# Kernel optimization log

Measured on AMD Instinct MI355X. Metric: run time of the kernel, lower is better.

The kernel has to match this reference:

```python
import jax, jax.numpy as jnp
import numpy as np

A = -0.75  # PyTorch bicubic coefficient (a=-0.75)


def _cubic_taps(n):
    # output coord i maps to src = i/2 - 0.25 (align_corners=False, scale=2)
    i = np.arange(2 * n)
    src = i / 2.0 - 0.25
    base = np.floor(src).astype(np.int64)
    t = src - base
    offs = np.array([-1, 0, 1, 2])
    idx = np.clip(base[:, None] + offs[None, :], 0, n - 1)  # (2n,4) replicate border
    d = np.abs(t[:, None] - offs[None, :])
    w = np.where(d <= 1.0,
                 (A + 2) * d ** 3 - (A + 3) * d ** 2 + 1.0,
                 A * d ** 3 - 5 * A * d ** 2 + 8 * A * d - 4 * A)
    return jnp.asarray(idx), jnp.asarray(w.astype(np.float32))


def _upsample2_bicubic(x):
    B, C, H, W = x.shape
    ih, wh = _cubic_taps(H)
    iw, ww = _cubic_taps(W)
    x = (x[:, :, ih, :] * wh[None, None, :, :, None]).sum(3)   # (B,C,2H,W)
    x = (x[:, :, :, iw] * ww[None, None, None, :, :]).sum(4)   # (B,C,2H,2W)
    return x


def _conv2d(x, w, b, pad):
    y = jax.lax.conv_general_dilated(x, w, (1, 1), ((pad, pad), (pad, pad)),
                                     dimension_numbers=('NCHW', 'OIHW', 'NCHW'))
    return y + b[None, :, None, None]


def _instance_norm(x, w, b, eps=1e-5):
    m = x.mean(axis=(2, 3), keepdims=True)
    v = x.var(axis=(2, 3), keepdims=True)
    return (x - m) * jax.lax.rsqrt(v + eps) * w[None, :, None, None] + b[None, :, None, None]


def _prelu(x, a):
    return jnp.where(x >= 0, x, a * x)


def _unfold5(x):
    # 5x5 neighborhoods, pad=2 -> (B, C, 25, H, W); row-major kernel tap order
    B, C, H, W = x.shape
    xp = jnp.pad(x, ((0, 0), (0, 0), (2, 2), (2, 2)))
    return jnp.stack([xp[:, :, i:i + H, j:j + W] for i in range(5) for j in range(5)], axis=2)


def _forward(input, feature, conv1_w, conv1_b, in1_w, in1_b, prelu1_a,
             conv2_w, conv2_b, in2_w, in2_b, prelu2_a,
             res_w, res_b, feat_w, feat_b, pac_w, pac_b):
    # main mapping: conv-IN-PReLU x2
    y = _prelu(_instance_norm(_conv2d(input, conv1_w, conv1_b, 1), in1_w, in1_b), prelu1_a)
    y = _prelu(_instance_norm(_conv2d(y, conv2_w, conv2_b, 1), in2_w, in2_b), prelu2_a)
    # residual 1x1 mapping (in_channels != out_channels)
    y = y + _conv2d(input, res_w, res_b, 0)
    y = _upsample2_bicubic(y)                               # (B,O,2H,2W)
    # PAC guidance: gaussian kernel from 1x1-mapped feature, normalized over window
    g = _conv2d(feature, feat_w, feat_b, 0)                 # (B,O,2H,2W)
    gcols = _unfold5(g)                                     # (B,O,25,2H,2W)
    diff2 = ((gcols - g[:, :, None]) ** 2).sum(axis=1)      # (B,25,2H,2W)
    kern = jnp.exp(-0.5 * diff2)
    kern = kern / kern.sum(axis=1, keepdims=True)           # normalize_kernel=True
    xcols = _unfold5(y)                                     # (B,O,25,2H,2W)
    O, Ci = pac_w.shape[0], pac_w.shape[1]
    out = jnp.einsum('ocp,bcphw,bphw->bohw', pac_w.reshape(O, Ci, 25), xcols, kern)
    return out + pac_b[None, :, None, None]


def setup_inputs() -> dict:
    key = jax.random.key(0)
    ks = jax.random.split(key, 8)
    Cin, Cout, Cf = 256, 128, 128
    B, H, W = 2, 48, 48
    f32 = jnp.float32

    def w(k, shape, fan_in):
        return jax.random.normal(k, shape, f32) / np.float32(np.sqrt(fan_in))

    return {
        'input': jax.random.normal(ks[0], (B, Cin, H, W), f32),
        'feature': jax.random.normal(ks[1], (B, Cf, 2 * H, 2 * W), f32),
        'conv1_w': w(ks[2], (Cout, Cin, 3, 3), Cin * 9), 'conv1_b': jnp.zeros((Cout,), f32),
        'in1_w': jnp.ones((Cout,), f32), 'in1_b': jnp.zeros((Cout,), f32),
        'prelu1_a': jnp.asarray(0.25, f32),
        'conv2_w': w(ks[3], (Cout, Cout, 3, 3), Cout * 9), 'conv2_b': jnp.zeros((Cout,), f32),
        'in2_w': jnp.ones((Cout,), f32), 'in2_b': jnp.zeros((Cout,), f32),
        'prelu2_a': jnp.asarray(0.25, f32),
        'res_w': w(ks[4], (Cout, Cin, 1, 1), Cin), 'res_b': jnp.zeros((Cout,), f32),
        'feat_w': w(ks[5], (Cout, Cf, 1, 1), Cf), 'feat_b': jnp.zeros((Cout,), f32),
        'pac_w': w(ks[6], (Cout, Cout, 5, 5), Cout * 25), 'pac_b': jnp.zeros((Cout,), f32),
    }


def reference(input, feature, conv1_w, conv1_b, in1_w, in1_b, prelu1_a,
              conv2_w, conv2_b, in2_w, in2_b, prelu2_a,
              res_w, res_b, feat_w, feat_b, pac_w, pac_b):
    return _forward(input, feature, conv1_w, conv1_b, in1_w, in1_b, prelu1_a,
                    conv2_w, conv2_b, in2_w, in2_b, prelu2_a,
                    res_w, res_b, feat_w, feat_b, pac_w, pac_b)
```

## Files before the change

### kernel.cpp

```cpp
#include <hip/hip_runtime.h>
#include <hip/hip_bf16.h>

typedef __attribute__((ext_vector_type(8))) short bf16x8;
typedef __attribute__((ext_vector_type(4))) float f32x4;

constexpr int B   = 2;
constexpr int CIN = 256;
constexpr int CO  = 128;
constexpr int H = 48, W = 48;
constexpr int H2 = 96, W2 = 96;
constexpr int NPIX1 = H * W;
constexpr int NPIX2 = H2 * W2;
constexpr int NS = 4;

__device__ inline ushort f2bf(float v)
{
  __hip_bfloat16 h = __float2bfloat16(v);
  return *reinterpret_cast<ushort*>(&h);
}

__global__ __launch_bounds__(256) void prep_weights_kernel(
    const float* __restrict__ pac_w, const float* __restrict__ conv1_w,
    const float* __restrict__ conv2_w, const float* __restrict__ feat_w,
    const float* __restrict__ res_w,
    ushort* __restrict__ wbb, ushort* __restrict__ wt1, ushort* __restrict__ wt2,
    ushort* __restrict__ fwb, ushort* __restrict__ wrb)
{
  int blk = blockIdx.x, tid = threadIdx.x;
  if (blk < 1600) {
    int idx = blk * 256 + tid;
    int c = idx & 127, o = (idx >> 7) & 127, p = idx >> 14;
    wbb[idx] = f2bf(pac_w[((size_t)o * CO + c) * 25 + p]);
  } else if (blk < 2752) {
    int idx = (blk - 1600) * 256 + tid;
    int ci = idx & 255, o = (idx >> 8) & 127, tap = idx >> 15;
    wt1[idx] = f2bf(conv1_w[((size_t)o * CIN + ci) * 9 + tap]);
  } else if (blk < 3328) {
    int idx = (blk - 2752) * 256 + tid;
    int ci = idx & 127, o = (idx >> 7) & 127, tap = idx >> 14;
    wt2[idx] = f2bf(conv2_w[((size_t)o * CO + ci) * 9 + tap]);
  } else if (blk < 3392) {
    int idx = (blk - 3328) * 256 + tid;
    fwb[idx] = f2bf(feat_w[idx]);
  } else {
    int idx = (blk - 3392) * 256 + tid;
    wrb[idx] = f2bf(res_w[idx]);
  }
}

__global__ __launch_bounds__(256) void cvt_in_t_kernel(
    const float* __restrict__ in, ushort* __restrict__ outh)
{
  int blk = blockIdx.x;
  int cg = blk & 7;
  int pc = (blk >> 3) % 36;
  int b  = blk / (8 * 36);
  int c0 = cg * 32, pix0 = pc * 64;
  int tid = threadIdx.x;
  __shared__ float lt[32][65];
#pragma unroll
  for (int r = 0; r < 8; r++) {
    int c_l = r * 4 + (tid >> 6), px = tid & 63;
    lt[c_l][px] = in[((size_t)b * CIN + c0 + c_l) * NPIX1 + pix0 + px];
  }
  __syncthreads();
  int c_l = tid & 31;
#pragma unroll
  for (int r = 0; r < 8; r++) {
    int px = r * 8 + (tid >> 5);
    outh[((size_t)b * NPIX1 + pix0 + px) * CIN + c0 + c_l] = f2bf(lt[c_l][px]);
  }
}

__global__ __launch_bounds__(256) void cvt_feat_t_kernel(
    const float* __restrict__ in, ushort* __restrict__ outh)
{
  int blk = blockIdx.x;
  int cg = blk & 3;
  int pc = (blk >> 2) % 144;
  int b  = blk / (4 * 144);
  int c0 = cg * 32, pix0 = pc * 64;
  int tid = threadIdx.x;
  __shared__ float lt[32][65];
#pragma unroll
  for (int r = 0; r < 8; r++) {
    int c_l = r * 4 + (tid >> 6), px = tid & 63;
    lt[c_l][px] = in[((size_t)b * CO + c0 + c_l) * NPIX2 + pix0 + px];
  }
  __syncthreads();
  int c_l = tid & 31;
#pragma unroll
  for (int r = 0; r < 8; r++) {
    int px = r * 8 + (tid >> 5);
    outh[((size_t)b * NPIX2 + pix0 + px) * CO + c0 + c_l] = f2bf(lt[c_l][px]);
  }
}

template<int CIg>
__global__ __launch_bounds__(256, 4) void conv3_mfma_kernel(
    const ushort* __restrict__ xh,
    const ushort* __restrict__ wt,
    float* __restrict__ pout)
{
  constexpr int CS = CIg / NS;
  constexpr int G  = CS / 8;
  constexpr int KC = CS / 32;
  int blk = blockIdx.x;
  int tile = blk % 36;
  int s = (blk / 36) & 3;
  int b = blk / 144;
  int th = tile / 3, tw = tile % 3;
  int h0 = th * 4, w0 = tw * 16;
  int tid = threadIdx.x, lane = tid & 63, wv = tid >> 6;
  int l15 = lane & 15, l4 = (lane >> 4) & 3;

  __shared__ ushort xt[108 * CS];
  for (int q = tid; q < 108 * G; q += 256) {
    int pixi = q / G, g = q & (G - 1);
    int rh = pixi / 18, rw = pixi - rh * 18;
    int hg = h0 - 1 + rh, wg = w0 - 1 + rw;
    uint4 v{0u, 0u, 0u, 0u};
    if (hg >= 0 && hg < H && wg >= 0 && wg < W)
      v = *(const uint4*)(xh + (size_t)(b * NPIX1 + hg * W + wg) * CIg + s * CS + g * 8);
    *(uint4*)(xt + pixi * CS + ((g ^ (pixi & (G - 1))) * 8)) = v;
  }
  __syncthreads();

  int wo = wv * 32;
  const ushort* wbase = wt + (size_t)(wo + l15) * CIg + s * CS + l4 * 8;

  f32x4 acc0[4], acc1[4];
#pragma unroll
  for (int nf = 0; nf < 4; nf++) {
    acc0[nf] = {0.f, 0.f, 0.f, 0.f};
    acc1[nf] = {0.f, 0.f, 0.f, 0.f};
  }

  bf16x8 aC0[KC], aC1[KC], aN0[KC], aN1[KC];
#pragma unroll
  for (int kc = 0; kc < KC; kc++) {
    aC0[kc] = *(const bf16x8*)(wbase + kc * 32);
    aC1[kc] = *(const bf16x8*)(wbase + 16 * CIg + kc * 32);
  }

#pragma unroll 1
  for (int tap = 0; tap < 9; ++tap) {
    if (tap < 8) {
      const ushort* wn = wbase + (size_t)(tap + 1) * 128 * CIg;
#pragma unroll
      for (int kc = 0; kc < KC; kc++) {
        aN0[kc] = *(const bf16x8*)(wn + kc * 32);
        aN1[kc] = *(const bf16x8*)(wn + 16 * CIg + kc * 32);
      }
    }
    int kh = (tap >= 6) ? 2 : ((tap >= 3) ? 1 : 0);
    int kw = tap - kh * 3;
#pragma unroll
    for (int kc = 0; kc < KC; kc++) {
#pragma unroll
      for (int nf = 0; nf < 4; nf++) {
        int pix = (nf + kh) * 18 + kw + l15;
        bf16x8 bb = *(const bf16x8*)(xt + pix * CS + (((kc * 4 + l4) ^ (pix & (G - 1))) * 8));
        acc0[nf] = __builtin_amdgcn_mfma_f32_16x16x32_bf16(aC0[kc], bb, acc0[nf], 0, 0, 0);
        acc1[nf] = __builtin_amdgcn_mfma_f32_16x16x32_bf16(aC1[kc], bb, acc1[nf], 0, 0, 0);
      }
    }
#pragma unroll
    for (int kc = 0; kc < KC; kc++) { aC0[kc] = aN0[kc]; aC1[kc] = aN1[kc]; }
  }

#pragma unroll
  for (int nf = 0; nf < 4; nf++) {
    int pixg = (h0 + nf) * W + w0 + l15;
#pragma unroll
    for (int r = 0; r < 4; r++) {
      int o = wo + l4 * 4 + r;
      pout[((size_t)(s * B + b) * CO + o) * NPIX1 + pixg] = acc0[nf][r];
      pout[((size_t)(s * B + b) * CO + o + 16) * NPIX1 + pixg] = acc1[nf][r];
    }
  }
}

__global__ __launch_bounds__(256) void reduce1_stats_kernel(
    const float* __restrict__ pout, const float* __restrict__ inw,
    const float* __restrict__ inb, float* __restrict__ scsh,
    float* __restrict__ outred)
{
  int bc = blockIdx.x, tid = threadIdx.x, c = bc & 127;
  float s = 0.f, s2 = 0.f;
#pragma unroll
  for (int i = 0; i < 9; i++) {
    size_t base = (size_t)bc * NPIX1 + tid + i * 256;
    float x = pout[base];
#pragma unroll
    for (int k = 1; k < NS; k++) x += pout[(size_t)k * B * CO * NPIX1 + base];
    outred[base] = x;
    s += x; s2 += x * x;
  }
#pragma unroll
  for (int off = 32; off > 0; off >>= 1) {
    s  += __shfl_down(s, off);
    s2 += __shfl_down(s2, off);
  }
  __shared__ float rs[4], rs2[4];
  int wid = tid >> 6, lane = tid & 63;
  if (lane == 0) { rs[wid] = s; rs2[wid] = s2; }
  __syncthreads();
  if (tid == 0) {
    float S  = rs[0] + rs[1] + rs[2] + rs[3];
    float S2 = rs2[0] + rs2[1] + rs2[2] + rs2[3];
    float mean = S * (1.f / NPIX1);
    float var  = S2 * (1.f / NPIX1) - mean * mean;
    float inv  = rsqrtf(var + 1e-5f);
    float sc = inw[c] * inv;
    scsh[2 * bc]     = sc;
    scsh[2 * bc + 1] = inb[c] - mean * sc;
  }
}

__global__ __launch_bounds__(256) void in_apply_hwc_kernel(
    const float* __restrict__ red, const float* __restrict__ scsh,
    const float* __restrict__ alpha_p, ushort* __restrict__ outh)
{
  int blk = blockIdx.x;
  int cg = blk & 3;
  int pc = (blk >> 2) % 36;
  int b  = blk / (4 * 36);
  int c0 = cg * 32, pix0 = pc * 64;
  int tid = threadIdx.x;
  float a = *alpha_p;
  __shared__ float lt[32][65];
#pragma unroll
  for (int r = 0; r < 8; r++) {
    int c_l = r * 4 + (tid >> 6), px = tid & 63;
    float x = red[((size_t)b * CO + c0 + c_l) * NPIX1 + pix0 + px];
    float sc = scsh[2 * (b * CO + c0 + c_l)];
    float sh = scsh[2 * (b * CO + c0 + c_l) + 1];
    float o = x * sc + sh;
    lt[c_l][px] = (o >= 0.f) ? o : a * o;
  }
  __syncthreads();
  int c_l = tid & 31;
#pragma unroll
  for (int r = 0; r < 8; r++) {
    int px = r * 8 + (tid >> 5);
    outh[((size_t)b * NPIX1 + pix0 + px) * CO + c0 + c_l] = f2bf(lt[c_l][px]);
  }
}

__global__ __launch_bounds__(256) void reduce_in_prelu_kernel(
    const float* __restrict__ pout, const float* __restrict__ cbias,
    const float* __restrict__ inw, const float* __restrict__ inb,
    const float* __restrict__ alpha_p, const float* __restrict__ radd,
    float* __restrict__ outf)
{
  int bc = blockIdx.x, tid = threadIdx.x, c = bc & 127;
  float bia = cbias[c];
  float v[9];
  float s = 0.f, s2 = 0.f;
#pragma unroll
  for (int i = 0; i < 9; i++) {
    size_t base = (size_t)bc * NPIX1 + tid + i * 256;
    float x = pout[base];
#pragma unroll
    for (int k = 1; k < NS; k++) x += pout[(size_t)k * B * CO * NPIX1 + base];
    x += bia;
    v[i] = x; s += x; s2 += x * x;
  }
#pragma unroll
  for (int off = 32; off > 0; off >>= 1) {
    s  += __shfl_down(s, off);
    s2 += __shfl_down(s2, off);
  }
  __shared__ float rs[4], rs2[4];
  int wid = tid >> 6, lane = tid & 63;
  if (lane == 0) { rs[wid] = s; rs2[wid] = s2; }
  __syncthreads();
  float S  = rs[0] + rs[1] + rs[2] + rs[3];
  float S2 = rs2[0] + rs2[1] + rs2[2] + rs2[3];
  float mean = S * (1.f / NPIX1);
  float var  = S2 * (1.f / NPIX1) - mean * mean;
  float inv  = rsqrtf(var + 1e-5f);
  float sc = inw[c] * inv;
  float sh = inb[c] - mean * sc;
  float a = *alpha_p;
#pragma unroll
  for (int i = 0; i < 9; i++) {
    size_t base = (size_t)bc * NPIX1 + tid + i * 256;
    float o = v[i] * sc + sh;
    o = (o >= 0.f) ? o : a * o;
    outf[base] = o + radd[base];
  }
}

__global__ __launch_bounds__(256, 4) void gemm_res_kernel(
    const ushort* __restrict__ xh,
    const ushort* __restrict__ wrb,
    const float* __restrict__ bias, float* __restrict__ out)
{
  int blk = blockIdx.x;
  int pc = blk % 72;
  int b  = blk / 72;
  int pix0 = pc * 32;
  int tid = threadIdx.x, lane = tid & 63, wv = tid >> 6;
  int l15 = lane & 15, l4 = (lane >> 4) & 3;

  __shared__ ushort xt[32 * 256];
  for (int q = tid; q < 1024; q += 256) {
    int pixi = q >> 5, g = q & 31;
    uint4 v = *(const uint4*)(xh + (((size_t)b * NPIX1 + pix0 + pixi) << 8) + (g << 3));
    *(uint4*)(xt + (pixi << 8) + ((g ^ (pixi & 31)) << 3)) = v;
  }
  __syncthreads();

  int wo = wv * 32;
  const ushort* wbase = wrb + (size_t)(wo + l15) * CIN + l4 * 8;
  bf16x8 a0[8], a1[8];
#pragma unroll
  for (int kc = 0; kc < 8; kc++) {
    a0[kc] = *(const bf16x8*)(wbase + kc * 32);
    a1[kc] = *(const bf16x8*)(wbase + 16 * CIN + kc * 32);
  }
  f32x4 acc0[2], acc1[2];
#pragma unroll
  for (int nf = 0; nf < 2; nf++) {
    acc0[nf] = {0.f, 0.f, 0.f, 0.f};
    acc1[nf] = {0.f, 0.f, 0.f, 0.f};
  }
#pragma unroll
  for (int nf = 0; nf < 2; nf++) {
    int pix = nf * 16 + l15;
    int base = pix << 8;
    int sw = pix & 31;
#pragma unroll
    for (int kc = 0; kc < 8; kc++) {
      bf16x8 bb = *(const bf16x8*)(xt + base + ((((kc << 2) + l4) ^ sw) << 3));
      acc0[nf] = __builtin_amdgcn_mfma_f32_16x16x32_bf16(a0[kc], bb, acc0[nf], 0, 0, 0);
      acc1[nf] = __builtin_amdgcn_mfma_f32_16x16x32_bf16(a1[kc], bb, acc1[nf], 0, 0, 0);
    }
  }
#pragma unroll
  for (int nf = 0; nf < 2; nf++) {
    int gp = pix0 + nf * 16 + l15;
#pragma unroll
    for (int r = 0; r < 4; r++) {
      int o = wo + l4 * 4 + r;
      out[((size_t)b * CO + o) * NPIX1 + gp] = acc0[nf][r] + bias[o];
      out[((size_t)b * CO + o + 16) * NPIX1 + gp] = acc1[nf][r] + bias[o + 16];
    }
  }
}

__global__ __launch_bounds__(256, 4) void gemm1x1_kernel(
    const ushort* __restrict__ fh,
    const ushort* __restrict__ fwb,
    const float* __restrict__ bias, float* __restrict__ out)
{
  int blk = blockIdx.x;
  int pc = blk % 144;
  int b  = blk / 144;
  int pix0 = pc * 64;
  int tid = threadIdx.x, lane = tid & 63, wv = tid >> 6;
  int l15 = lane & 15, l4 = (lane >> 4) & 3;

  __shared__ ushort xt[64 * 128];
  for (int q = tid; q < 1024; q += 256) {
    int pixi = q >> 4, g = q & 15;
    uint4 v = *(const uint4*)(fh + (((size_t)b * NPIX2 + pix0 + pixi) << 7) + (g << 3));
    *(uint4*)(xt + (pixi << 7) + ((g ^ (pixi & 15)) << 3)) = v;
  }
  __syncthreads();

  int wo = wv * 32;
  const ushort* wbase = fwb + (size_t)(wo + l15) * CO + l4 * 8;
  bf16x8 a0[4], a1[4];
#pragma unroll
  for (int kc = 0; kc < 4; kc++) {
    a0[kc] = *(const bf16x8*)(wbase + kc * 32);
    a1[kc] = *(const bf16x8*)(wbase + 16 * CO + kc * 32);
  }
  f32x4 acc0[4], acc1[4];
#pragma unroll
  for (int nf = 0; nf < 4; nf++) {
    acc0[nf] = {0.f, 0.f, 0.f, 0.f};
    acc1[nf] = {0.f, 0.f, 0.f, 0.f};
  }
#pragma unroll
  for (int nf = 0; nf < 4; nf++) {
    int pix = nf * 16 + l15;
    int base = pix << 7;
    int sw = pix & 15;
#pragma unroll
    for (int kc = 0; kc < 4; kc++) {
      bf16x8 bb = *(const bf16x8*)(xt + base + ((((kc << 2) + l4) ^ sw) << 3));
      acc0[nf] = __builtin_amdgcn_mfma_f32_16x16x32_bf16(a0[kc], bb, acc0[nf], 0, 0, 0);
      acc1[nf] = __builtin_amdgcn_mfma_f32_16x16x32_bf16(a1[kc], bb, acc1[nf], 0, 0, 0);
    }
  }
#pragma unroll
  for (int nf = 0; nf < 4; nf++) {
    int gp = pix0 + nf * 16 + l15;
#pragma unroll
    for (int r = 0; r < 4; r++) {
      int o = wo + l4 * 4 + r;
      out[((size_t)b * CO + o) * NPIX2 + gp] = acc0[nf][r] + bias[o];
      out[((size_t)b * CO + o + 16) * NPIX2 + gp] = acc1[nf][r] + bias[o + 16];
    }
  }
}

__device__ inline void bicubic_taps(int i, int n, int* r, float* w)
{
  const float we[4] = {-0.03515625f, 0.26171875f, 0.87890625f, -0.10546875f};
  bool odd = (i & 1);
  int base = (i >> 1) + (odd ? 0 : -1);
#pragma unroll
  for (int q = 0; q < 4; q++) {
    int rr = base + q - 1;
    r[q] = rr < 0 ? 0 : (rr > n - 1 ? n - 1 : rr);
    w[q] = odd ? we[3 - q] : we[q];
  }
}

__global__ __launch_bounds__(256) void upsample_t_kernel(
    const float* __restrict__ in, ushort* __restrict__ outh)
{
  int blk = blockIdx.x;
  int cg = blk & 3;
  int i  = (blk >> 2) % H2;
  int b  = blk / (4 * H2);
  int c0 = cg * 32;
  int tid = threadIdx.x;

  int rh[4]; float wh[4];
  bicubic_taps(i, H, rh, wh);

  __shared__ float ls[4 * 48 * 33];
  for (int k = 0; k < 24; k++) {
    int q = tid + k * 256;
    int ww = q % 48;
    int a  = (q / 48) & 3;
    int c_l = q / 192;
    ls[(a * 48 + ww) * 33 + c_l] =
        in[((size_t)b * CO + c0 + c_l) * NPIX1 + rh[a] * W + ww];
  }
  __syncthreads();

  int c_l = tid & 31;
#pragma unroll
  for (int rep = 0; rep < 12; rep++) {
    int j = rep * 8 + (tid >> 5);
    int rwj[4]; float wwj[4];
    bicubic_taps(j, W, rwj, wwj);
    float s = 0.f;
#pragma unroll
    for (int a = 0; a < 4; a++) {
      float r = 0.f;
#pragma unroll
      for (int q = 0; q < 4; q++)
        r += wwj[q] * ls[(a * 48 + rwj[q]) * 33 + c_l];
      s += wh[a] * r;
    }
    outh[((size_t)(b * H2 + i) * W2 + j) * CO + c0 + c_l] = f2bf(s);
  }
}

__global__ __launch_bounds__(256) void pac_kern_part_kernel(
    const float* __restrict__ g, float* __restrict__ pd2)
{
  int blk = blockIdx.x;
  int s = blk & 3;
  int tile = (blk >> 2) % 36;
  int b = blk / (4 * 36);
  int ty = tile / 6, tx = tile % 6;
  int h0 = ty * 16, w0 = tx * 16;
  int tid = threadIdx.x, px = tid & 15, py = tid >> 4;
  __shared__ float gt[8][20 * 24];
  float d2[25];
#pragma unroll
  for (int p = 0; p < 25; p++) d2[p] = 0.f;

  int cbase = s * 32;
#pragma unroll 1
  for (int cc = 0; cc < 32; cc += 8) {
    for (int idx = tid; idx < 3200; idx += 256) {
      int c_l = idx / 400, r = idx - c_l * 400;
      int rh = r / 20, rw = r - rh * 20;
      int hh = h0 - 2 + rh, ww = w0 - 2 + rw;
      float v = 0.f;
      if (hh >= 0 && hh < H2 && ww >= 0 && ww < W2)
        v = g[((size_t)b * CO + cbase + cc + c_l) * NPIX2 + hh * W2 + ww];
      gt[c_l][rh * 24 + rw] = v;
    }
    __syncthreads();
#pragma unroll
    for (int c_l = 0; c_l < 8; c_l++) {
      float ctr = gt[c_l][(py + 2) * 24 + px + 2];
#pragma unroll
      for (int dy = 0; dy < 5; dy++)
#pragma unroll
        for (int dx = 0; dx < 5; dx++) {
          float d = gt[c_l][(py + dy) * 24 + px + dx] - ctr;
          d2[dy * 5 + dx] += d * d;
        }
    }
    __syncthreads();
  }
  float* op = pd2 + ((size_t)((b * 36 + tile) * 4 + s) * 25) * 256 + tid;
#pragma unroll
  for (int p = 0; p < 25; p++) op[(size_t)p * 256] = d2[p];
}

__global__ __launch_bounds__(256) void pac_kern_fin_kernel(
    const float* __restrict__ pd2, float* __restrict__ kern)
{
  int blk = blockIdx.x;
  int tile = blk % 36, b = blk / 36;
  int ty = tile / 6, tx = tile % 6;
  int h0 = ty * 16, w0 = tx * 16;
  int tid = threadIdx.x, px = tid & 15, py = tid >> 4;
  const float* ip = pd2 + ((size_t)(b * 36 + tile) * 4 * 25) * 256 + tid;
  float e[25];
  float sum = 0.f;
#pragma unroll
  for (int p = 0; p < 25; p++) {
    float d = 0.f;
#pragma unroll
    for (int s = 0; s < 4; s++) d += ip[(size_t)(s * 25 + p) * 256];
    e[p] = __expf(-0.5f * d);
    sum += e[p];
  }
  float inv = 1.f / sum;
  int pixg = (h0 + py) * W2 + w0 + px;
  float* op = kern + ((size_t)b * NPIX2 + pixg) * 32;
#pragma unroll
  for (int p = 0; p < 25; p++) op[p] = e[p] * inv;
}

__global__ __launch_bounds__(256, 2) void pac_mfma_kernel(
    const ushort* __restrict__ xh,
    const float* __restrict__ kern,
    const ushort* __restrict__ wb,
    const float* __restrict__ bias, float* __restrict__ out)
{
  int blk = blockIdx.x;
  int og = blk & 1;
  int tw = (blk >> 1) % 6;
  int th = (blk >> 1) / 6 % 12;
  int b  = blk / (2 * 6 * 12);
  int h0 = th * 8, w0 = tw * 16;
  int tid = threadIdx.x, lane = tid & 63, wv = tid >> 6;
  int l15 = lane & 15, l4 = (lane >> 4) & 3;

  __shared__ ushort xt[240 * 128];
  __shared__ float kt[128][33];

  for (int q = tid; q < 3840; q += 256) {
    int pixi = q >> 4, cb = q & 15;
    int rh = pixi / 20, rw = pixi - rh * 20;
    int hg = h0 - 2 + rh, wg = w0 - 2 + rw;
    uint4 v{0u, 0u, 0u, 0u};
    if (hg >= 0 && hg < H2 && wg >= 0 && wg < W2)
      v = *(const uint4*)(xh + ((((size_t)b * H2 + hg) * W2 + wg) << 7) + (cb << 3));
    *(uint4*)(xt + (pixi << 7) + ((cb ^ (pixi & 15)) << 3)) = v;
  }
  for (int q = tid; q < 1024; q += 256) {
    int pixl = q >> 3, poff = (q & 7) << 2;
    int r = pixl >> 4, col = pixl & 15;
    const float* kp = kern + ((size_t)b * NPIX2 + (h0 + r) * W2 + w0 + col) * 32 + poff;
    float4 kv = *(const float4*)kp;
    kt[pixl][poff] = kv.x; kt[pixl][poff + 1] = kv.y;
    kt[pixl][poff + 2] = kv.z; kt[pixl][poff + 3] = kv.w;
  }
  __syncthreads();

  int wo = og * 64 + wv * 16;
  const ushort* wbase = wb + (size_t)(wo + l15) * CO + l4 * 8;

  f32x4 acc[8];
#pragma unroll
  for (int nf = 0; nf < 8; nf++) acc[nf] = {0.f, 0.f, 0.f, 0.f};

  bf16x8 aC[4], aN[4];
#pragma unroll
  for (int kc = 0; kc < 4; kc++)
    aC[kc] = *(const bf16x8*)(wbase + kc * 32);

  int dy = 0, dx = 0;
#pragma unroll 1
  for (int p = 0; p < 25; ++p) {
    if (p < 24) {
      const ushort* wnext = wbase + (size_t)(p + 1) * CO * CO;
#pragma unroll
      for (int kc = 0; kc < 4; kc++)
        aN[kc] = *(const bf16x8*)(wnext + kc * 32);
    }
#pragma unroll
    for (int nf = 0; nf < 8; nf++) {
      int pix = (nf + dy) * 20 + dx + l15;
      int base = pix << 7;
      int sw = pix & 15;
      f32x4 y = {0.f, 0.f, 0.f, 0.f};
#pragma unroll
      for (int kc = 0; kc < 4; kc++) {
        bf16x8 bb = *(const bf16x8*)(xt + base + (((kc * 4 + l4) ^ sw) << 3));
        y = __builtin_amdgcn_mfma_f32_16x16x32_bf16(aC[kc], bb, y, 0, 0, 0);
      }
      float ks = kt[(nf << 4) + l15][p];
#pragma unroll
      for (int r = 0; r < 4; r++) acc[nf][r] += ks * y[r];
    }
#pragma unroll
    for (int kc = 0; kc < 4; kc++) aC[kc] = aN[kc];
    if (++dx == 5) { dx = 0; dy++; }
  }

#pragma unroll
  for (int nf = 0; nf < 8; nf++) {
    int gpix = (h0 + nf) * W2 + w0 + l15;
#pragma unroll
    for (int r = 0; r < 4; r++) {
      int o = wo + l4 * 4 + r;
      out[((size_t)b * CO + o) * NPIX2 + gpix] = acc[nf][r] + bias[o];
    }
  }
}

extern "C" void kernel_launch(void* const* d_in, const int* in_sizes, int n_in,
                              void* d_out, int out_size, void* d_ws, size_t ws_size,
                              hipStream_t stream)
{
  (void)in_sizes; (void)n_in; (void)out_size; (void)ws_size;
  const float* input    = (const float*)d_in[0];
  const float* feature  = (const float*)d_in[1];
  const float* conv1_w  = (const float*)d_in[2];
  const float* conv1_b  = (const float*)d_in[3];
  const float* in1_w    = (const float*)d_in[4];
  const float* in1_b    = (const float*)d_in[5];
  const float* prelu1_a = (const float*)d_in[6];
  const float* conv2_w  = (const float*)d_in[7];
  const float* conv2_b  = (const float*)d_in[8];
  const float* in2_w    = (const float*)d_in[9];
  const float* in2_b    = (const float*)d_in[10];
  const float* prelu2_a = (const float*)d_in[11];
  const float* res_w    = (const float*)d_in[12];
  const float* res_b    = (const float*)d_in[13];
  const float* feat_w   = (const float*)d_in[14];
  const float* feat_b   = (const float*)d_in[15];
  const float* pac_w    = (const float*)d_in[16];
  const float* pac_b    = (const float*)d_in[17];
  float* out = (float*)d_out;

  float* ws = (float*)d_ws;
  float*  kern = ws;
  ushort* t1h  = (ushort*)ws;
  ushort* wt2  = (ushort*)(ws + 294912);
  ushort* wt1  = (ushort*)(ws + 368640);
  float*  t2   = ws + 589824;
  float*  pws  = ws + 1179648;
  float*  g    = ws + 3538944;
  ushort* xinh = (ushort*)g;
  ushort* yh   = (ushort*)(ws + 5898240);
  ushort* wbb  = (ushort*)(ws + 7077888);
  float*  scsh = ws + 7282688;
  ushort* fh   = (ushort*)(ws + 7283200);
  ushort* fwb  = (ushort*)(ws + 8462848);
  ushort* wrb  = (ushort*)(ws + 8471040);
  float*  radd = ws + 8487424;
  float*  pd2  = pws;

  prep_weights_kernel<<<3520, 256, 0, stream>>>(
      pac_w, conv1_w, conv2_w, feat_w, res_w, wbb, wt1, wt2, fwb, wrb);
  cvt_in_t_kernel<<<B * 36 * 8, 256, 0, stream>>>(input, xinh);
  cvt_feat_t_kernel<<<B * 144 * 4, 256, 0, stream>>>(feature, fh);

  conv3_mfma_kernel<CIN><<<B * NS * 36, 256, 0, stream>>>(xinh, wt1, pws);
  reduce1_stats_kernel<<<B * CO, 256, 0, stream>>>(pws, in1_w, in1_b, scsh, t2);
  in_apply_hwc_kernel<<<B * 36 * 4, 256, 0, stream>>>(t2, scsh, prelu1_a, t1h);
  gemm_res_kernel<<<B * 72, 256, 0, stream>>>(xinh, wrb, res_b, radd);
  conv3_mfma_kernel<CO><<<B * NS * 36, 256, 0, stream>>>(t1h, wt2, pws);
  reduce_in_prelu_kernel<<<B * CO, 256, 0, stream>>>(
      pws, conv2_b, in2_w, in2_b, prelu2_a, radd, t2);
  upsample_t_kernel<<<B * H2 * 4, 256, 0, stream>>>(t2, yh);
  gemm1x1_kernel<<<B * 144, 256, 0, stream>>>(fh, fwb, feat_b, g);
  pac_kern_part_kernel<<<B * 36 * 4, 256, 0, stream>>>(g, pd2);
  pac_kern_fin_kernel<<<B * 36, 256, 0, stream>>>(pd2, kern);
  pac_mfma_kernel<<<B * 12 * 6 * 2, 256, 0, stream>>>(yh, kern, wbb, pac_b, out);
}
```

Before: 144.6 us.

## Horizontally fuse independent kernels into combined launches to fill the GPU

Merges the two input transposes into one launch, and combines conv1 with the residual 1x1 GEMM and the feature 1x1 GEMM in one grid. It also runs conv2 alongside the PAC kernel distance partials, and the second instance-norm reduce alongside the kernel softmax finalize. This cuts launch count and lets small, independent grids fill more CUs at once. Workspace buffers that previously aliased (xinh/g, pd2/pws) get separate regions so concurrent blocks do not clobber each other, at the cost of more workspace memory and larger shared allocations for the smaller branches.

```diff
diff --git a/kernel.cpp b/kernel.cpp
--- a/kernel.cpp
+++ b/kernel.cpp
@@ -48,73 +48,69 @@
   }
 }
 
-__global__ __launch_bounds__(256) void cvt_in_t_kernel(
-    const float* __restrict__ in, ushort* __restrict__ outh)
-{
-  int blk = blockIdx.x;
-  int cg = blk & 7;
-  int pc = (blk >> 3) % 36;
-  int b  = blk / (8 * 36);
-  int c0 = cg * 32, pix0 = pc * 64;
+__global__ __launch_bounds__(256) void cvt_both_kernel(
+    const float* __restrict__ input, const float* __restrict__ feature,
+    ushort* __restrict__ xinh, ushort* __restrict__ fh)
+{
+  __shared__ float lt[32][65];
   int tid = threadIdx.x;
-  __shared__ float lt[32][65];
-#pragma unroll
-  for (int r = 0; r < 8; r++) {
-    int c_l = r * 4 + (tid >> 6), px = tid & 63;
-    lt[c_l][px] = in[((size_t)b * CIN + c0 + c_l) * NPIX1 + pix0 + px];
-  }
-  __syncthreads();
-  int c_l = tid & 31;
-#pragma unroll
-  for (int r = 0; r < 8; r++) {
-    int px = r * 8 + (tid >> 5);
-    outh[((size_t)b * NPIX1 + pix0 + px) * CIN + c0 + c_l] = f2bf(lt[c_l][px]);
-  }
-}
-
-__global__ __launch_bounds__(256) void cvt_feat_t_kernel(
-    const float* __restrict__ in, ushort* __restrict__ outh)
-{
-  int blk = blockIdx.x;
-  int cg = blk & 3;
-  int pc = (blk >> 2) % 144;
-  int b  = blk / (4 * 144);
-  int c0 = cg * 32, pix0 = pc * 64;
-  int tid = threadIdx.x;
-  __shared__ float lt[32][65];
-#pragma unroll
-  for (int r = 0; r < 8; r++) {
-    int c_l = r * 4 + (tid >> 6), px = tid & 63;
-    lt[c_l][px] = in[((size_t)b * CO + c0 + c_l) * NPIX2 + pix0 + px];
-  }
-  __syncthreads();
-  int c_l = tid & 31;
-#pragma unroll
-  for (int r = 0; r < 8; r++) {
-    int px = r * 8 + (tid >> 5);
-    outh[((size_t)b * NPIX2 + pix0 + px) * CO + c0 + c_l] = f2bf(lt[c_l][px]);
+  if (blockIdx.x < 576) {
+    int blk = blockIdx.x;
+    int cg = blk & 7;
+    int pc = (blk >> 3) % 36;
+    int b  = blk / (8 * 36);
+    int c0 = cg * 32, pix0 = pc * 64;
+#pragma unroll
+    for (int r = 0; r < 8; r++) {
+      int c_l = r * 4 + (tid >> 6), px = tid & 63;
+      lt[c_l][px] = input[((size_t)b * CIN + c0 + c_l) * NPIX1 + pix0 + px];
+    }
+    __syncthreads();
+    int c_l = tid & 31;
+#pragma unroll
+    for (int r = 0; r < 8; r++) {
+      int px = r * 8 + (tid >> 5);
+      xinh[((size_t)b * NPIX1 + pix0 + px) * CIN + c0 + c_l] = f2bf(lt[c_l][px]);
+    }
+  } else {
+    int blk = blockIdx.x - 576;
+    int cg = blk & 3;
+    int pc = (blk >> 2) % 144;
+    int b  = blk / (4 * 144);
+    int c0 = cg * 32, pix0 = pc * 64;
+#pragma unroll
+    for (int r = 0; r < 8; r++) {
+      int c_l = r * 4 + (tid >> 6), px = tid & 63;
+      lt[c_l][px] = feature[((size_t)b * CO + c0 + c_l) * NPIX2 + pix0 + px];
+    }
+    __syncthreads();
+    int c_l = tid & 31;
+#pragma unroll
+    for (int r = 0; r < 8; r++) {
+      int px = r * 8 + (tid >> 5);
+      fh[((size_t)b * NPIX2 + pix0 + px) * CO + c0 + c_l] = f2bf(lt[c_l][px]);
+    }
   }
 }
 
 template<int CIg>
-__global__ __launch_bounds__(256, 4) void conv3_mfma_kernel(
-    const ushort* __restrict__ xh,
-    const ushort* __restrict__ wt,
+__device__ __forceinline__ void conv3_body(
+    int blk, int tid, char* smraw,
+    const ushort* __restrict__ xh, const ushort* __restrict__ wt,
     float* __restrict__ pout)
 {
   constexpr int CS = CIg / NS;
   constexpr int G  = CS / 8;
   constexpr int KC = CS / 32;
-  int blk = blockIdx.x;
+  ushort* xt = (ushort*)smraw;
   int tile = blk % 36;
   int s = (blk / 36) & 3;
   int b = blk / 144;
   int th = tile / 3, tw = tile % 3;
   int h0 = th * 4, w0 = tw * 16;
-  int tid = threadIdx.x, lane = tid & 63, wv = tid >> 6;
+  int lane = tid & 63, wv = tid >> 6;
   int l15 = lane & 15, l4 = (lane >> 4) & 3;
 
-  __shared__ ushort xt[108 * CS];
   for (int q = tid; q < 108 * G; q += 256) {
     int pixi = q / G, g = q & (G - 1);
     int rh = pixi / 18, rw = pixi - rh * 18;
@@ -179,6 +175,276 @@
       pout[((size_t)(s * B + b) * CO + o + 16) * NPIX1 + pixg] = acc1[nf][r];
     }
   }
+}
+
+__device__ __forceinline__ void gemm_res_body(
+    int blk, int tid, char* smraw,
+    const ushort* __restrict__ xh, const ushort* __restrict__ wrb,
+    const float* __restrict__ bias, float* __restrict__ out)
+{
+  ushort* xt = (ushort*)smraw;
+  int pc = blk % 72;
+  int b  = blk / 72;
+  int pix0 = pc * 32;
+  int lane = tid & 63, wv = tid >> 6;
+  int l15 = lane & 15, l4 = (lane >> 4) & 3;
+
+  for (int q = tid; q < 1024; q += 256) {
+    int pixi = q >> 5, g = q & 31;
+    uint4 v = *(const uint4*)(xh + (((size_t)b * NPIX1 + pix0 + pixi) << 8) + (g << 3));
+    *(uint4*)(xt + (pixi << 8) + ((g ^ (pixi & 31)) << 3)) = v;
+  }
+  __syncthreads();
+
+  int wo = wv * 32;
+  const ushort* wbase = wrb + (size_t)(wo + l15) * CIN + l4 * 8;
+  bf16x8 a0[8], a1[8];
+#pragma unroll
+  for (int kc = 0; kc < 8; kc++) {
+    a0[kc] = *(const bf16x8*)(wbase + kc * 32);
+    a1[kc] = *(const bf16x8*)(wbase + 16 * CIN + kc * 32);
+  }
+  f32x4 acc0[2], acc1[2];
+#pragma unroll
+  for (int nf = 0; nf < 2; nf++) {
+    acc0[nf] = {0.f, 0.f, 0.f, 0.f};
+    acc1[nf] = {0.f, 0.f, 0.f, 0.f};
+  }
+#pragma unroll
+  for (int nf = 0; nf < 2; nf++) {
+    int pix = nf * 16 + l15;
+    int base = pix << 8;
+    int sw = pix & 31;
+#pragma unroll
+    for (int kc = 0; kc < 8; kc++) {
+      bf16x8 bb = *(const bf16x8*)(xt + base + ((((kc << 2) + l4) ^ sw) << 3));
+      acc0[nf] = __builtin_amdgcn_mfma_f32_16x16x32_bf16(a0[kc], bb, acc0[nf], 0, 0, 0);
+      acc1[nf] = __builtin_amdgcn_mfma_f32_16x16x32_bf16(a1[kc], bb, acc1[nf], 0, 0, 0);
+    }
+  }
+#pragma unroll
+  for (int nf = 0; nf < 2; nf++) {
+    int gp = pix0 + nf * 16 + l15;
+#pragma unroll
+    for (int r = 0; r < 4; r++) {
+      int o = wo + l4 * 4 + r;
+      out[((size_t)b * CO + o) * NPIX1 + gp] = acc0[nf][r] + bias[o];
+      out[((size_t)b * CO + o + 16) * NPIX1 + gp] = acc1[nf][r] + bias[o + 16];
+    }
+  }
+}
+
+__device__ __forceinline__ void gemm1x1_body(
+    int blk, int tid, char* smraw,
+    const ushort* __restrict__ fh, const ushort* __restrict__ fwb,
+    const float* __restrict__ bias, float* __restrict__ out)
+{
+  ushort* xt = (ushort*)smraw;
+  int pc = blk % 144;
+  int b  = blk / 144;
+  int pix0 = pc * 64;
+  int lane = tid & 63, wv = tid >> 6;
+  int l15 = lane & 15, l4 = (lane >> 4) & 3;
+
+  for (int q = tid; q < 1024; q += 256) {
+    int pixi = q >> 4, g = q & 15;
+    uint4 v = *(const uint4*)(fh + (((size_t)b * NPIX2 + pix0 + pixi) << 7) + (g << 3));
+    *(uint4*)(xt + (pixi << 7) + ((g ^ (pixi & 15)) << 3)) = v;
+  }
+  __syncthreads();
+
+  int wo = wv * 32;
+  const ushort* wbase = fwb + (size_t)(wo + l15) * CO + l4 * 8;
+  bf16x8 a0[4], a1[4];
+#pragma unroll
+  for (int kc = 0; kc < 4; kc++) {
+    a0[kc] = *(const bf16x8*)(wbase + kc * 32);
+    a1[kc] = *(const bf16x8*)(wbase + 16 * CO + kc * 32);
+  }
+  f32x4 acc0[4], acc1[4];
+#pragma unroll
+  for (int nf = 0; nf < 4; nf++) {
+    acc0[nf] = {0.f, 0.f, 0.f, 0.f};
+    acc1[nf] = {0.f, 0.f, 0.f, 0.f};
+  }
+#pragma unroll
+  for (int nf = 0; nf < 4; nf++) {
+    int pix = nf * 16 + l15;
+    int base = pix << 7;
+    int sw = pix & 15;
+#pragma unroll
+    for (int kc = 0; kc < 4; kc++) {
+      bf16x8 bb = *(const bf16x8*)(xt + base + ((((kc << 2) + l4) ^ sw) << 3));
+      acc0[nf] = __builtin_amdgcn_mfma_f32_16x16x32_bf16(a0[kc], bb, acc0[nf], 0, 0, 0);
+      acc1[nf] = __builtin_amdgcn_mfma_f32_16x16x32_bf16(a1[kc], bb, acc1[nf], 0, 0, 0);
+    }
+  }
+#pragma unroll
+  for (int nf = 0; nf < 4; nf++) {
+    int gp = pix0 + nf * 16 + l15;
+#pragma unroll
+    for (int r = 0; r < 4; r++) {
+      int o = wo + l4 * 4 + r;
+      out[((size_t)b * CO + o) * NPIX2 + gp] = acc0[nf][r] + bias[o];
+      out[((size_t)b * CO + o + 16) * NPIX2 + gp] = acc1[nf][r] + bias[o + 16];
+    }
+  }
+}
+
+__global__ __launch_bounds__(256, 4) void mega1_kernel(
+    const ushort* __restrict__ xinh, const ushort* __restrict__ wt1,
+    float* __restrict__ pws,
+    const ushort* __restrict__ wrb, const float* __restrict__ res_b,
+    float* __restrict__ radd,
+    const ushort* __restrict__ fh, const ushort* __restrict__ fwb,
+    const float* __restrict__ feat_b, float* __restrict__ g)
+{
+  __shared__ __align__(16) char sm[16384];
+  int blk = blockIdx.x, tid = threadIdx.x;
+  if (blk < 288)      conv3_body<CIN>(blk, tid, sm, xinh, wt1, pws);
+  else if (blk < 432) gemm_res_body(blk - 288, tid, sm, xinh, wrb, res_b, radd);
+  else                gemm1x1_body(blk - 432, tid, sm, fh, fwb, feat_b, g);
+}
+
+__device__ __forceinline__ void kern_part_body(
+    int blk, int tid, char* smraw,
+    const float* __restrict__ g, float* __restrict__ pd2)
+{
+  float (*gt)[480] = (float(*)[480])smraw;
+  int s = blk & 3;
+  int tile = (blk >> 2) % 36;
+  int b = blk / (4 * 36);
+  int ty = tile / 6, tx = tile % 6;
+  int h0 = ty * 16, w0 = tx * 16;
+  int px = tid & 15, py = tid >> 4;
+  float d2[25];
+#pragma unroll
+  for (int p = 0; p < 25; p++) d2[p] = 0.f;
+
+  int cbase = s * 32;
+#pragma unroll 1
+  for (int cc = 0; cc < 32; cc += 8) {
+    for (int idx = tid; idx < 3200; idx += 256) {
+      int c_l = idx / 400, r = idx - c_l * 400;
+      int rh = r / 20, rw = r - rh * 20;
+      int hh = h0 - 2 + rh, ww = w0 - 2 + rw;
+      float v = 0.f;
+      if (hh >= 0 && hh < H2 && ww >= 0 && ww < W2)
+        v = g[((size_t)b * CO + cbase + cc + c_l) * NPIX2 + hh * W2 + ww];
+      gt[c_l][rh * 24 + rw] = v;
+    }
+    __syncthreads();
+#pragma unroll
+    for (int c_l = 0; c_l < 8; c_l++) {
+      float ctr = gt[c_l][(py + 2) * 24 + px + 2];
+#pragma unroll
+      for (int dy = 0; dy < 5; dy++)
+#pragma unroll
+        for (int dx = 0; dx < 5; dx++) {
+          float d = gt[c_l][(py + dy) * 24 + px + dx] - ctr;
+          d2[dy * 5 + dx] += d * d;
+        }
+    }
+    __syncthreads();
+  }
+  float* op = pd2 + ((size_t)((b * 36 + tile) * 4 + s) * 25) * 256 + tid;
+#pragma unroll
+  for (int p = 0; p < 25; p++) op[(size_t)p * 256] = d2[p];
+}
+
+__global__ __launch_bounds__(256, 4) void mega2_kernel(
+    const ushort* __restrict__ t1h, const ushort* __restrict__ wt2,
+    float* __restrict__ pws,
+    const float* __restrict__ g, float* __restrict__ pd2)
+{
+  __shared__ __align__(16) char sm[15360];
+  int blk = blockIdx.x, tid = threadIdx.x;
+  if (blk < 288) conv3_body<CO>(blk, tid, sm, t1h, wt2, pws);
+  else           kern_part_body(blk - 288, tid, sm, g, pd2);
+}
+
+__device__ __forceinline__ void reduce2_body(
+    int bc, int tid,
+    const float* __restrict__ pout, const float* __restrict__ cbias,
+    const float* __restrict__ inw, const float* __restrict__ inb,
+    const float* __restrict__ alpha_p, const float* __restrict__ radd,
+    float* __restrict__ outf)
+{
+  int c = bc & 127;
+  float bia = cbias[c];
+  float v[9];
+  float s = 0.f, s2 = 0.f;
+#pragma unroll
+  for (int i = 0; i < 9; i++) {
+    size_t base = (size_t)bc * NPIX1 + tid + i * 256;
+    float x = pout[base];
+#pragma unroll
+    for (int k = 1; k < NS; k++) x += pout[(size_t)k * B * CO * NPIX1 + base];
+    x += bia;
+    v[i] = x; s += x; s2 += x * x;
+  }
+#pragma unroll
+  for (int off = 32; off > 0; off >>= 1) {
+    s  += __shfl_down(s, off);
+    s2 += __shfl_down(s2, off);
+  }
+  __shared__ float rs[4], rs2[4];
+  int wid = tid >> 6, lane = tid & 63;
+  if (lane == 0) { rs[wid] = s; rs2[wid] = s2; }
+  __syncthreads();
+  float S  = rs[0] + rs[1] + rs[2] + rs[3];
+  float S2 = rs2[0] + rs2[1] + rs2[2] + rs2[3];
+  float mean = S * (1.f / NPIX1);
+  float var  = S2 * (1.f / NPIX1) - mean * mean;
+  float inv  = rsqrtf(var + 1e-5f);
+  float sc = inw[c] * inv;
+  float sh = inb[c] - mean * sc;
+  float a = *alpha_p;
+#pragma unroll
+  for (int i = 0; i < 9; i++) {
+    size_t base = (size_t)bc * NPIX1 + tid + i * 256;
+    float o = v[i] * sc + sh;
+    o = (o >= 0.f) ? o : a * o;
+    outf[base] = o + radd[base];
+  }
+}
+
+__device__ __forceinline__ void kern_fin_body(
+    int blk, int tid,
+    const float* __restrict__ pd2, float* __restrict__ kern)
+{
+  int tile = blk % 36, b = blk / 36;
+  int ty = tile / 6, tx = tile % 6;
+  int h0 = ty * 16, w0 = tx * 16;
+  int px = tid & 15, py = tid >> 4;
+  const float* ip = pd2 + ((size_t)(b * 36 + tile) * 4 * 25) * 256 + tid;
+  float e[25];
+  float sum = 0.f;
+#pragma unroll
+  for (int p = 0; p < 25; p++) {
+    float d = 0.f;
+#pragma unroll
+    for (int s = 0; s < 4; s++) d += ip[(size_t)(s * 25 + p) * 256];
+    e[p] = __expf(-0.5f * d);
+    sum += e[p];
+  }
+  float inv = 1.f / sum;
+  int pixg = (h0 + py) * W2 + w0 + px;
+  float* op = kern + ((size_t)b * NPIX2 + pixg) * 32;
+#pragma unroll
+  for (int p = 0; p < 25; p++) op[p] = e[p] * inv;
+}
+
+__global__ __launch_bounds__(256) void mega3_kernel(
+    const float* __restrict__ pws, const float* __restrict__ conv2_b,
+    const float* __restrict__ in2_w, const float* __restrict__ in2_b,
+    const float* __restrict__ prelu2_a, const float* __restrict__ radd,
+    float* __restrict__ t2,
+    const float* __restrict__ pd2, float* __restrict__ kern)
+{
+  int blk = blockIdx.x, tid = threadIdx.x;
+  if (blk < 256) reduce2_body(blk, tid, pws, conv2_b, in2_w, in2_b, prelu2_a, radd, t2);
+  else           kern_fin_body(blk - 256, tid, pd2, kern);
 }
 
 __global__ __launch_bounds__(256) void reduce1_stats_kernel(
@@ -248,167 +514,6 @@
   }
 }
 
-__global__ __launch_bounds__(256) void reduce_in_prelu_kernel(
-    const float* __restrict__ pout, const float* __restrict__ cbias,
-    const float* __restrict__ inw, const float* __restrict__ inb,
-    const float* __restrict__ alpha_p, const float* __restrict__ radd,
-    float* __restrict__ outf)
-{
-  int bc = blockIdx.x, tid = threadIdx.x, c = bc & 127;
-  float bia = cbias[c];
-  float v[9];
-  float s = 0.f, s2 = 0.f;
-#pragma unroll
-  for (int i = 0; i < 9; i++) {
-    size_t base = (size_t)bc * NPIX1 + tid + i * 256;
-    float x = pout[base];
-#pragma unroll
-    for (int k = 1; k < NS; k++) x += pout[(size_t)k * B * CO * NPIX1 + base];
-    x += bia;
-    v[i] = x; s += x; s2 += x * x;
-  }
-#pragma unroll
-  for (int off = 32; off > 0; off >>= 1) {
-    s  += __shfl_down(s, off);
-    s2 += __shfl_down(s2, off);
-  }
-  __shared__ float rs[4], rs2[4];
-  int wid = tid >> 6, lane = tid & 63;
-  if (lane == 0) { rs[wid] = s; rs2[wid] = s2; }
-  __syncthreads();
-  float S  = rs[0] + rs[1] + rs[2] + rs[3];
-  float S2 = rs2[0] + rs2[1] + rs2[2] + rs2[3];
-  float mean = S * (1.f / NPIX1);
-  float var  = S2 * (1.f / NPIX1) - mean * mean;
-  float inv  = rsqrtf(var + 1e-5f);
-  float sc = inw[c] * inv;
-  float sh = inb[c] - mean * sc;
-  float a = *alpha_p;
-#pragma unroll
-  for (int i = 0; i < 9; i++) {
-    size_t base = (size_t)bc * NPIX1 + tid + i * 256;
-    float o = v[i] * sc + sh;
-    o = (o >= 0.f) ? o : a * o;
-    outf[base] = o + radd[base];
-  }
-}
-
-__global__ __launch_bounds__(256, 4) void gemm_res_kernel(
-    const ushort* __restrict__ xh,
-    const ushort* __restrict__ wrb,
-    const float* __restrict__ bias, float* __restrict__ out)
-{
-  int blk = blockIdx.x;
-  int pc = blk % 72;
-  int b  = blk / 72;
-  int pix0 = pc * 32;
-  int tid = threadIdx.x, lane = tid & 63, wv = tid >> 6;
-  int l15 = lane & 15, l4 = (lane >> 4) & 3;
-
-  __shared__ ushort xt[32 * 256];
-  for (int q = tid; q < 1024; q += 256) {
-    int pixi = q >> 5, g = q & 31;
-    uint4 v = *(const uint4*)(xh + (((size_t)b * NPIX1 + pix0 + pixi) << 8) + (g << 3));
-    *(uint4*)(xt + (pixi << 8) + ((g ^ (pixi & 31)) << 3)) = v;
-  }
-  __syncthreads();
-
-  int wo = wv * 32;
-  const ushort* wbase = wrb + (size_t)(wo + l15) * CIN + l4 * 8;
-  bf16x8 a0[8], a1[8];
-#pragma unroll
-  for (int kc = 0; kc < 8; kc++) {
-    a0[kc] = *(const bf16x8*)(wbase + kc * 32);
-    a1[kc] = *(const bf16x8*)(wbase + 16 * CIN + kc * 32);
-  }
-  f32x4 acc0[2], acc1[2];
-#pragma unroll
-  for (int nf = 0; nf < 2; nf++) {
-    acc0[nf] = {0.f, 0.f, 0.f, 0.f};
-    acc1[nf] = {0.f, 0.f, 0.f, 0.f};
-  }
-#pragma unroll
-  for (int nf = 0; nf < 2; nf++) {
-    int pix = nf * 16 + l15;
-    int base = pix << 8;
-    int sw = pix & 31;
-#pragma unroll
-    for (int kc = 0; kc < 8; kc++) {
-      bf16x8 bb = *(const bf16x8*)(xt + base + ((((kc << 2) + l4) ^ sw) << 3));
-      acc0[nf] = __builtin_amdgcn_mfma_f32_16x16x32_bf16(a0[kc], bb, acc0[nf], 0, 0, 0);
-      acc1[nf] = __builtin_amdgcn_mfma_f32_16x16x32_bf16(a1[kc], bb, acc1[nf], 0, 0, 0);
-    }
-  }
-#pragma unroll
-  for (int nf = 0; nf < 2; nf++) {
-    int gp = pix0 + nf * 16 + l15;
-#pragma unroll
-    for (int r = 0; r < 4; r++) {
-      int o = wo + l4 * 4 + r;
-      out[((size_t)b * CO + o) * NPIX1 + gp] = acc0[nf][r] + bias[o];
-      out[((size_t)b * CO + o + 16) * NPIX1 + gp] = acc1[nf][r] + bias[o + 16];
-    }
-  }
-}
-
-__global__ __launch_bounds__(256, 4) void gemm1x1_kernel(
-    const ushort* __restrict__ fh,
-    const ushort* __restrict__ fwb,
-    const float* __restrict__ bias, float* __restrict__ out)
-{
-  int blk = blockIdx.x;
-  int pc = blk % 144;
-  int b  = blk / 144;
-  int pix0 = pc * 64;
-  int tid = threadIdx.x, lane = tid & 63, wv = tid >> 6;
-  int l15 = lane & 15, l4 = (lane >> 4) & 3;
-
-  __shared__ ushort xt[64 * 128];
-  for (int q = tid; q < 1024; q += 256) {
-    int pixi = q >> 4, g = q & 15;
-    uint4 v = *(const uint4*)(fh + (((size_t)b * NPIX2 + pix0 + pixi) << 7) + (g << 3));
-    *(uint4*)(xt + (pixi << 7) + ((g ^ (pixi & 15)) << 3)) = v;
-  }
-  __syncthreads();
-
-  int wo = wv * 32;
-  const ushort* wbase = fwb + (size_t)(wo + l15) * CO + l4 * 8;
-  bf16x8 a0[4], a1[4];
-#pragma unroll
-  for (int kc = 0; kc < 4; kc++) {
-    a0[kc] = *(const bf16x8*)(wbase + kc * 32);
-    a1[kc] = *(const bf16x8*)(wbase + 16 * CO + kc * 32);
-  }
-  f32x4 acc0[4], acc1[4];
-#pragma unroll
-  for (int nf = 0; nf < 4; nf++) {
-    acc0[nf] = {0.f, 0.f, 0.f, 0.f};
-    acc1[nf] = {0.f, 0.f, 0.f, 0.f};
-  }
-#pragma unroll
-  for (int nf = 0; nf < 4; nf++) {
-    int pix = nf * 16 + l15;
-    int base = pix << 7;
-    int sw = pix & 15;
-#pragma unroll
-    for (int kc = 0; kc < 4; kc++) {
-      bf16x8 bb = *(const bf16x8*)(xt + base + ((((kc << 2) + l4) ^ sw) << 3));
-      acc0[nf] = __builtin_amdgcn_mfma_f32_16x16x32_bf16(a0[kc], bb, acc0[nf], 0, 0, 0);
-      acc1[nf] = __builtin_amdgcn_mfma_f32_16x16x32_bf16(a1[kc], bb, acc1[nf], 0, 0, 0);
-    }
-  }
-#pragma unroll
-  for (int nf = 0; nf < 4; nf++) {
-    int gp = pix0 + nf * 16 + l15;
-#pragma unroll
-    for (int r = 0; r < 4; r++) {
-      int o = wo + l4 * 4 + r;
-      out[((size_t)b * CO + o) * NPIX2 + gp] = acc0[nf][r] + bias[o];
-      out[((size_t)b * CO + o + 16) * NPIX2 + gp] = acc1[nf][r] + bias[o + 16];
-    }
-  }
-}
-
 __device__ inline void bicubic_taps(int i, int n, int* r, float* w)
 {
   const float we[4] = {-0.03515625f, 0.26171875f, 0.87890625f, -0.10546875f};
@@ -463,78 +568,6 @@
     }
     outh[((size_t)(b * H2 + i) * W2 + j) * CO + c0 + c_l] = f2bf(s);
   }
-}
-
-__global__ __launch_bounds__(256) void pac_kern_part_kernel(
-    const float* __restrict__ g, float* __restrict__ pd2)
-{
-  int blk = blockIdx.x;
-  int s = blk & 3;
-  int tile = (blk >> 2) % 36;
-  int b = blk / (4 * 36);
-  int ty = tile / 6, tx = tile % 6;
-  int h0 = ty * 16, w0 = tx * 16;
-  int tid = threadIdx.x, px = tid & 15, py = tid >> 4;
-  __shared__ float gt[8][20 * 24];
-  float d2[25];
-#pragma unroll
-  for (int p = 0; p < 25; p++) d2[p] = 0.f;
-
-  int cbase = s * 32;
-#pragma unroll 1
-  for (int cc = 0; cc < 32; cc += 8) {
-    for (int idx = tid; idx < 3200; idx += 256) {
-      int c_l = idx / 400, r = idx - c_l * 400;
-      int rh = r / 20, rw = r - rh * 20;
-      int hh = h0 - 2 + rh, ww = w0 - 2 + rw;
-      float v = 0.f;
-      if (hh >= 0 && hh < H2 && ww >= 0 && ww < W2)
-        v = g[((size_t)b * CO + cbase + cc + c_l) * NPIX2 + hh * W2 + ww];
-      gt[c_l][rh * 24 + rw] = v;
-    }
-    __syncthreads();
-#pragma unroll
-    for (int c_l = 0; c_l < 8; c_l++) {
-      float ctr = gt[c_l][(py + 2) * 24 + px + 2];
-#pragma unroll
-      for (int dy = 0; dy < 5; dy++)
-#pragma unroll
-        for (int dx = 0; dx < 5; dx++) {
-          float d = gt[c_l][(py + dy) * 24 + px + dx] - ctr;
-          d2[dy * 5 + dx] += d * d;
-        }
-    }
-    __syncthreads();
-  }
-  float* op = pd2 + ((size_t)((b * 36 + tile) * 4 + s) * 25) * 256 + tid;
-#pragma unroll
-  for (int p = 0; p < 25; p++) op[(size_t)p * 256] = d2[p];
-}
-
-__global__ __launch_bounds__(256) void pac_kern_fin_kernel(
-    const float* __restrict__ pd2, float* __restrict__ kern)
-{
-  int blk = blockIdx.x;
-  int tile = blk % 36, b = blk / 36;
-  int ty = tile / 6, tx = tile % 6;
-  int h0 = ty * 16, w0 = tx * 16;
-  int tid = threadIdx.x, px = tid & 15, py = tid >> 4;
-  const float* ip = pd2 + ((size_t)(b * 36 + tile) * 4 * 25) * 256 + tid;
-  float e[25];
-  float sum = 0.f;
-#pragma unroll
-  for (int p = 0; p < 25; p++) {
-    float d = 0.f;
-#pragma unroll
-    for (int s = 0; s < 4; s++) d += ip[(size_t)(s * 25 + p) * 256];
-    e[p] = __expf(-0.5f * d);
-    sum += e[p];
-  }
-  float inv = 1.f / sum;
-  int pixg = (h0 + py) * W2 + w0 + px;
-  float* op = kern + ((size_t)b * NPIX2 + pixg) * 32;
-#pragma unroll
-  for (int p = 0; p < 25; p++) op[p] = e[p] * inv;
 }
 
 __global__ __launch_bounds__(256, 2) void pac_mfma_kernel(
@@ -667,23 +700,20 @@
   ushort* fwb  = (ushort*)(ws + 8462848);
   ushort* wrb  = (ushort*)(ws + 8471040);
   float*  radd = ws + 8487424;
-  float*  pd2  = pws;
+  float*  pd2  = ws + 9077248;
+  ushort* xinh2 = (ushort*)(ws + 10920448);
 
   prep_weights_kernel<<<3520, 256, 0, stream>>>(
       pac_w, conv1_w, conv2_w, feat_w, res_w, wbb, wt1, wt2, fwb, wrb);
-  cvt_in_t_kernel<<<B * 36 * 8, 256, 0, stream>>>(input, xinh);
-  cvt_feat_t_kernel<<<B * 144 * 4, 256, 0, stream>>>(feature, fh);
-
-  conv3_mfma_kernel<CIN><<<B * NS * 36, 256, 0, stream>>>(xinh, wt1, pws);
+  cvt_both_kernel<<<1728, 256, 0, stream>>>(input, feature, xinh2, fh);
+
+  mega1_kernel<<<720, 256, 0, stream>>>(
+      xinh2, wt1, pws, wrb, res_b, radd, fh, fwb, feat_b, g);
   reduce1_stats_kernel<<<B * CO, 256, 0, stream>>>(pws, in1_w, in1_b, scsh, t2);
   in_apply_hwc_kernel<<<B * 36 * 4, 256, 0, stream>>>(t2, scsh, prelu1_a, t1h);
-  gemm_res_kernel<<<B * 72, 256, 0, stream>>>(xinh, wrb, res_b, radd);
-  conv3_mfma_kernel<CO><<<B * NS * 36, 256, 0, stream>>>(t1h, wt2, pws);
-  reduce_in_prelu_kernel<<<B * CO, 256, 0, stream>>>(
-      pws, conv2_b, in2_w, in2_b, prelu2_a, radd, t2);
+  mega2_kernel<<<576, 256, 0, stream>>>(t1h, wt2, pws, g, pd2);
+  mega3_kernel<<<328, 256, 0, stream>>>(
+      pws, conv2_b, in2_w, in2_b, prelu2_a, radd, t2, pd2, kern);
   upsample_t_kernel<<<B * H2 * 4, 256, 0, stream>>>(t2, yh);
-  gemm1x1_kernel<<<B * 144, 256, 0, stream>>>(fh, fwb, feat_b, g);
-  pac_kern_part_kernel<<<B * 36 * 4, 256, 0, stream>>>(g, pd2);
-  pac_kern_fin_kernel<<<B * 36, 256, 0, stream>>>(pd2, kern);
   pac_mfma_kernel<<<B * 12 * 6 * 2, 256, 0, stream>>>(yh, kern, wbb, pac_b, out);
 }
```

After: 123.9 us. 14.3% less time.
